# Kernel optimization log

Hardware: AMD Instinct MI355X
Metric: run time of the kernel (lower is better)

Reference implementation:

```python
import jax, jax.numpy as jnp
import numpy as np

N_QUBITS = 12
N_LAYERS = 5
DIM = 1 << N_QUBITS            # 4096
N3 = 3 * N_QUBITS              # 36 params per rotation layer
N_PARAM = N3 * (N_LAYERS + 1)  # 216
BATCH = 1024
# he_std * lrmul with gain=sqrt(2), use_wscale=True, lrmul=1 -> w_mul = sqrt(2/5), init_std = 1
W_SCALE = (2.0 ** 0.5) * (5.0 ** -0.5)
TWO_PI = 2.0 * np.pi

CNOT = jnp.array([[1, 0, 0, 0],
                  [0, 1, 0, 0],
                  [0, 0, 0, 1],
                  [0, 0, 1, 0]], dtype=jnp.complex64)


def setup_inputs() -> dict:
    key = jax.random.key(0)
    k1, k2 = jax.random.split(key)
    x = jax.random.normal(k1, (BATCH, DIM), dtype=jnp.float32)
    weight = (jax.random.uniform(k2, (N_PARAM,), dtype=jnp.float32,
                                 minval=0.0, maxval=TWO_PI) * W_SCALE)
    return {"x": x, "weight": weight}


def _rx(t):
    c = jnp.cos(0.5 * t).astype(jnp.complex64)
    s = jnp.sin(0.5 * t).astype(jnp.complex64)
    return jnp.stack([jnp.stack([c, -1j * s]), jnp.stack([-1j * s, c])])


def _ry(t):
    c = jnp.cos(0.5 * t).astype(jnp.complex64)
    s = jnp.sin(0.5 * t).astype(jnp.complex64)
    return jnp.stack([jnp.stack([c, -s]), jnp.stack([s, c])])


def _rz(t):
    e = jnp.exp(-0.5j * t.astype(jnp.complex64))
    z = jnp.zeros((), dtype=jnp.complex64)
    return jnp.stack([jnp.stack([e, z]), jnp.stack([z, jnp.conj(e)])])


def _apply1(state, U, q):
    # state: [B, 2, ..., 2]; apply 2x2 gate U on qubit axis q
    state = jnp.moveaxis(state, 1 + q, -1)
    state = jnp.einsum('ab,...b->...a', U, state)
    return jnp.moveaxis(state, -1, 1 + q)


def _apply2(state, U, q0, q1):
    # apply 4x4 gate U on (control q0, target q1)
    state = jnp.moveaxis(state, (1 + q0, 1 + q1), (-2, -1))
    shp = state.shape
    state = state.reshape(shp[:-2] + (4,))
    state = jnp.einsum('ab,...b->...a', U, state)
    state = state.reshape(shp)
    return jnp.moveaxis(state, (-2, -1), (1 + q0, 1 + q1))


def reference(x, weight):
    # amplitude_encoding (faithful to source: divides by sqrt(norm), norm = ||x||)
    norm = jnp.sqrt(jnp.sum(x * x, axis=-1, keepdims=True))
    psi = (x / jnp.sqrt(norm + 1e-12)).astype(jnp.complex64)
    state = psi.reshape((x.shape[0],) + (2,) * N_QUBITS)

    for l in range(N_LAYERS):
        p = weight[l * N3:(l + 1) * N3].reshape(N_QUBITS, 3)
        # XYZLayer: rx, ry, rz per qubit (fused into one 2x2 per qubit)
        for q in range(N_QUBITS):
            U = _rz(p[q, 2]) @ _ry(p[q, 1]) @ _rx(p[q, 0])
            state = _apply1(state, U, q)
        # ring_of_cnot
        for q in range(N_QUBITS):
            state = _apply2(state, CNOT, q, (q + 1) % N_QUBITS)

    # final YZYLayer: ry, rz, ry per qubit
    p = weight[N_LAYERS * N3:].reshape(N_QUBITS, 3)
    for q in range(N_QUBITS):
        U = _ry(p[q, 2]) @ _rz(p[q, 1]) @ _ry(p[q, 0])
        state = _apply1(state, U, q)

    res = state.reshape(x.shape[0], DIM)
    return jnp.real(res)
```

## Files before the change

### kernel.cpp

```cpp
#include <hip/hip_runtime.h>
#include <math.h>

#define NQ 12
#define NLAYERS 5
#define TPB 256

typedef float v4f __attribute__((ext_vector_type(4)));
typedef short v8s __attribute__((ext_vector_type(8)));

#define MFMA(A, B, C) __builtin_amdgcn_mfma_f32_16x16x32_bf16((A), (B), (C), 0, 0, 0)

__device__ __forceinline__ float2 cmulf(float2 a, float2 b) {
    return make_float2(a.x * b.x - a.y * b.y, a.x * b.y + a.y * b.x);
}
__device__ __forceinline__ float2 caddf(float2 a, float2 b) {
    return make_float2(a.x + b.x, a.y + b.y);
}
__device__ __forceinline__ void mat2mul(const float2 A[4], const float2 B[4], float2 C[4]) {
    C[0] = caddf(cmulf(A[0], B[0]), cmulf(A[1], B[2]));
    C[1] = caddf(cmulf(A[0], B[1]), cmulf(A[1], B[3]));
    C[2] = caddf(cmulf(A[2], B[0]), cmulf(A[3], B[2]));
    C[3] = caddf(cmulf(A[2], B[1]), cmulf(A[3], B[3]));
}

__device__ __forceinline__ v8s pk4(unsigned a, unsigned b, unsigned c, unsigned d) {
    union { unsigned u[4]; v8s s; } x;
    x.u[0] = a; x.u[1] = b; x.u[2] = c; x.u[3] = d;
    return x.s;
}
__device__ __forceinline__ unsigned cvt2(float a, float b) {
    unsigned d;
    asm("v_cvt_pk_bf16_f32 %0, %1, %2" : "=v"(d) : "v"(a), "v"(b));
    return d;
}
__device__ __forceinline__ unsigned packhl_rne(float f) {
    unsigned h = cvt2(f, 0.0f);
    float lo = f - __uint_as_float(h << 16);
    unsigned l = cvt2(lo, 0.0f);
    return h | (l << 16);
}

__device__ __forceinline__ int sx4(int x) { x ^= x >> 1; x ^= x >> 2; return x & 15; }
__device__ __forceinline__ int permR(int row) {
    int s = sx4(row), par = s & 1;
    return ((s ^ (par << 3)) << 8) | (par ? 0xFF : 0);
}
__device__ __forceinline__ int permT(int t) {
    int s = sx4(t), par = s & 1;
    return (par << 11) | (s << 4) | (par ? 0xF : 0);
}
__device__ __forceinline__ int permL(int lo) {
    int s = sx4(lo), par = s & 1;
    return s | (par << 11);
}

__device__ __forceinline__ int slotOf(int k) {
    int v = k >> 4, m = k & 15;
    int vk = v ^ (((v >> 3) ^ (v >> 7)) & 1);
    return (vk << 4) | ((((m >> 2) ^ v) & 3) << 2) | (m & 3);
}

__device__ __forceinline__ void buildW(const float2* gm, int layer, int beta, int tid,
                                       unsigned& wrd, unsigned& wid) {
    const int r = tid >> 4, c = tid & 15;
    float2 u = make_float2(1.f, 0.f);
    #pragma unroll
    for (int bb = 0; bb < 4; ++bb) {
        const float2 e = gm[(layer * 12 + 11 - beta - bb) * 4 + ((r >> bb) & 1) * 2 + ((c >> bb) & 1)];
        u = cmulf(u, e);
    }
    wrd = packhl_rne(u.x);
    wid = packhl_rne(u.y);
}

__device__ __forceinline__ void makeAfrags(const unsigned* wrR, const unsigned* wiR, int af,
                                           v8s& a_crh, v8s& a_crl, v8s& a_cih, v8s& a_cil) {
    const uint4 wr4 = *reinterpret_cast<const uint4*>(wrR + af);
    const uint4 wi4 = *reinterpret_cast<const uint4*>(wiR + af);
    const unsigned NX = 0x80008000u;
    const unsigned SLO = 0x05040100u, SHI = 0x07060302u;
    unsigned n0 = wi4.x ^ NX, n1 = wi4.y ^ NX, n2 = wi4.z ^ NX, n3 = wi4.w ^ NX;
    a_crh = pk4(__builtin_amdgcn_perm(n0, wr4.x, SLO), __builtin_amdgcn_perm(n1, wr4.y, SLO),
                __builtin_amdgcn_perm(n2, wr4.z, SLO), __builtin_amdgcn_perm(n3, wr4.w, SLO));
    a_crl = pk4(__builtin_amdgcn_perm(n0, wr4.x, SHI), __builtin_amdgcn_perm(n1, wr4.y, SHI),
                __builtin_amdgcn_perm(n2, wr4.z, SHI), __builtin_amdgcn_perm(n3, wr4.w, SHI));
    a_cih = pk4(__builtin_amdgcn_perm(wr4.x, wi4.x, SLO), __builtin_amdgcn_perm(wr4.y, wi4.y, SLO),
                __builtin_amdgcn_perm(wr4.z, wi4.z, SLO), __builtin_amdgcn_perm(wr4.w, wi4.w, SLO));
    a_cil = pk4(__builtin_amdgcn_perm(wr4.x, wi4.x, SHI), __builtin_amdgcn_perm(wr4.y, wi4.y, SHI),
                __builtin_amdgcn_perm(wr4.z, wi4.z, SHI), __builtin_amdgcn_perm(wr4.w, wi4.w, SHI));
}

__global__ __launch_bounds__(TPB) void qsim_kernel(const float* __restrict__ x,
                                                   const float* __restrict__ wgt,
                                                   float* __restrict__ out) {
    __shared__ __align__(16) unsigned st[2][4096];
    __shared__ __align__(16) unsigned wrp[2][256];
    __shared__ __align__(16) unsigned wip[2][256];
    __shared__ __align__(16) float2 gmat[288];
    __shared__ float red[4];

    const int tid = threadIdx.x;
    const int lane = tid & 63;
    const int w = tid >> 6;
    const int hl = lane >> 4;
    const int l15 = lane & 15;
    const int b = blockIdx.x;

    if (tid < 72) {
        const int l = tid / NQ;
        const int q = tid % NQ;
        const float* pp = wgt + (l < NLAYERS ? l * (3 * NQ) : NLAYERS * (3 * NQ)) + q * 3;
        float s0, c0, s1, c1, s2, c2;
        sincosf(0.5f * pp[0], &s0, &c0);
        sincosf(0.5f * pp[1], &s1, &c1);
        sincosf(0.5f * pp[2], &s2, &c2);
        float2 U[4], M[4];
        if (l < NLAYERS) {
            float2 RX[4] = { {c0, 0.f}, {0.f, -s0}, {0.f, -s0}, {c0, 0.f} };
            float2 RY[4] = { {c1, 0.f}, {-s1, 0.f}, {s1, 0.f}, {c1, 0.f} };
            float2 RZ[4] = { {c2, -s2}, {0.f, 0.f}, {0.f, 0.f}, {c2, s2} };
            mat2mul(RY, RX, M);
            mat2mul(RZ, M, U);
        } else {
            float2 RY0[4] = { {c0, 0.f}, {-s0, 0.f}, {s0, 0.f}, {c0, 0.f} };
            float2 RZ1[4] = { {c1, -s1}, {0.f, 0.f}, {0.f, 0.f}, {c1, s1} };
            float2 RY2[4] = { {c2, 0.f}, {-s2, 0.f}, {s2, 0.f}, {c2, 0.f} };
            mat2mul(RZ1, RY0, M);
            mat2mul(RY2, M, U);
        }
        gmat[tid * 4 + 0] = U[0];
        gmat[tid * 4 + 1] = U[1];
        gmat[tid * 4 + 2] = U[2];
        gmat[tid * 4 + 3] = U[3];
    }

    const float* xb = x + (size_t)b * 4096;
    float vals[16];
    float ss = 0.f;
    {
        const float4* xv = reinterpret_cast<const float4*>(xb + 16 * tid);
        #pragma unroll
        for (int k = 0; k < 4; ++k) {
            float4 v = xv[k];
            vals[k * 4 + 0] = v.x; vals[k * 4 + 1] = v.y;
            vals[k * 4 + 2] = v.z; vals[k * 4 + 3] = v.w;
            ss += v.x * v.x + v.y * v.y + v.z * v.z + v.w * v.w;
        }
    }
    #pragma unroll
    for (int off = 32; off > 0; off >>= 1) ss += __shfl_down(ss, off, 64);
    if (lane == 0) red[w] = ss;
    __syncthreads();

    const float total = red[0] + red[1] + red[2] + red[3];
    const float inv = 1.0f / sqrtf(sqrtf(total) + 1e-12f);

    const int vkT = tid ^ (((tid >> 3) ^ (tid >> 7)) & 1);
    #pragma unroll
    for (int jq = 0; jq < 4; ++jq) {
        const int base = (vkT << 4) | (((jq ^ tid) & 3) << 2);
        uint4 eq;
        eq.x = cvt2(vals[jq * 4 + 0] * inv, 0.f);
        eq.y = cvt2(vals[jq * 4 + 1] * inv, 0.f);
        eq.z = cvt2(vals[jq * 4 + 2] * inv, 0.f);
        eq.w = cvt2(vals[jq * 4 + 3] * inv, 0.f);
        *reinterpret_cast<uint4*>(&st[0][base]) = eq;
    }

    {
        unsigned wrd, wid;
        buildW(gmat, 0, 0, tid, wrd, wid);
        wrp[0][tid] = wrd; wip[0][tid] = wid;
    }

    const int v0 = (w << 6) | l15;
    const int vk0 = v0 ^ ((((v0 >> 3) ^ (v0 >> 7)) & 1));
    const int rbase = (vk0 << 4) | ((hl ^ (l15 & 3)) << 2);
    const int af = l15 * 16 + 4 * hl;
    int bw[4], pg[4], pt[4];
    const int sgb = slotOf((4 * hl) << 8);
    const int plc = slotOf(permL(l15));
    #pragma unroll
    for (int ti = 0; ti < 4; ++ti) {
        bw[ti] = sgb ^ slotOf((((4 * w + ti) << 4) | l15));
        pt[ti] = plc ^ slotOf(permT(4 * w + ti));
    }
    #pragma unroll
    for (int g = 0; g < 4; ++g) pg[g] = slotOf(permR(4 * hl + g));
    const int obase = ((4 * hl) << 8) | ((4 * w) << 4) | l15;
    float* outp = out + (size_t)b * 4096;

    __syncthreads();

    const v4f z = {0.f, 0.f, 0.f, 0.f};

    #pragma unroll 1
    for (int p = 0; p < 17; ++p) {
        const unsigned* __restrict__ stR = &st[p & 1][0];
        unsigned* __restrict__ stW = &st[(p + 1) & 1][0];

        v8s a_crh, a_crl, a_cih, a_cil;
        makeAfrags(&wrp[p & 1][0], &wip[p & 1][0], af, a_crh, a_crl, a_cih, a_cil);

        const uint4 s0 = *reinterpret_cast<const uint4*>(stR + rbase);
        const uint4 s1 = *reinterpret_cast<const uint4*>(stR + rbase + 256);
        const uint4 s2 = *reinterpret_cast<const uint4*>(stR + rbase + 512);
        const uint4 s3 = *reinterpret_cast<const uint4*>(stR + rbase + 768);

        unsigned ent[4][4];
        #pragma unroll
        for (int ti = 0; ti < 4; ++ti) {
            const uint4 sv = (ti == 0) ? s0 : (ti == 1) ? s1 : (ti == 2) ? s2 : s3;
            const v8s bsv = pk4(sv.x, sv.y, sv.z, sv.w);
            v4f cr = MFMA(a_crl, bsv, z);
            cr = MFMA(a_crh, bsv, cr);
            v4f ci = MFMA(a_cil, bsv, z);
            ci = MFMA(a_cih, bsv, ci);
            #pragma unroll
            for (int g = 0; g < 4; ++g)
                ent[ti][g] = cvt2(cr[g], ci[g]);
        }

        {
            const int pn = p + 1;
            unsigned wrd, wid;
            buildW(gmat, pn / 3, 4 * (pn % 3), tid, wrd, wid);
            wrp[pn & 1][tid] = wrd;
            wip[pn & 1][tid] = wid;
        }

        if (p % 3 == 2) {
            #pragma unroll
            for (int ti = 0; ti < 4; ++ti) {
                #pragma unroll
                for (int g = 0; g < 4; ++g)
                    stW[pg[g] ^ pt[ti]] = ent[ti][g];
            }
        } else {
            #pragma unroll
            for (int ti = 0; ti < 4; ++ti) {
                #pragma unroll
                for (int g = 0; g < 4; ++g)
                    stW[bw[ti] + (g << 8)] = ent[ti][g];
            }
        }
        __syncthreads();
    }

    {
        const unsigned* __restrict__ stR = &st[1][0];
        v8s a_crh, a_crl, a_cih, a_cil;
        makeAfrags(&wrp[1][0], &wip[1][0], af, a_crh, a_crl, a_cih, a_cil);
        #pragma unroll
        for (int ti = 0; ti < 4; ++ti) {
            const uint4 sv = *reinterpret_cast<const uint4*>(stR + rbase + ti * 256);
            const v8s bsv = pk4(sv.x, sv.y, sv.z, sv.w);
            v4f cr = MFMA(a_crl, bsv, z);
            cr = MFMA(a_crh, bsv, cr);
            #pragma unroll
            for (int g = 0; g < 4; ++g)
                outp[obase + (g << 8) + (ti << 4)] = cr[g];
        }
    }
}

extern "C" void kernel_launch(void* const* d_in, const int* in_sizes, int n_in,
                              void* d_out, int out_size, void* d_ws, size_t ws_size,
                              hipStream_t stream) {
    const float* x = (const float*)d_in[0];
    const float* wgt = (const float*)d_in[1];
    float* out = (float*)d_out;
    qsim_kernel<<<dim3(1024), dim3(TPB), 0, stream>>>(x, wgt, out);
}
```

Measured before the change: 35.80 us.

## Precompute packed gate matrices in a prep kernel and prefetch from global

Moves the per-block trig and 16x16 gate-matrix construction into a single-block prep kernel that writes all 18 packed bf16 matrices to workspace. The main kernel then loads each matrix fragment straight from global (L2-resident) memory, prefetching the next stage's fragment during the current stage. This removes the redundant per-block sincos and buildW work and the LDS traffic for the weight matrices. In exchange it adds a second kernel launch with a serial dependency, plus global-load latency inside the stage loop.

```diff
diff --git a/kernel.cpp b/kernel.cpp
--- a/kernel.cpp
+++ b/kernel.cpp
@@ -73,10 +73,8 @@
     wid = packhl_rne(u.y);
 }
 
-__device__ __forceinline__ void makeAfrags(const unsigned* wrR, const unsigned* wiR, int af,
+__device__ __forceinline__ void makeAfrags(uint4 wr4, uint4 wi4,
                                            v8s& a_crh, v8s& a_crl, v8s& a_cih, v8s& a_cil) {
-    const uint4 wr4 = *reinterpret_cast<const uint4*>(wrR + af);
-    const uint4 wi4 = *reinterpret_cast<const uint4*>(wiR + af);
     const unsigned NX = 0x80008000u;
     const unsigned SLO = 0x05040100u, SHI = 0x07060302u;
     unsigned n0 = wi4.x ^ NX, n1 = wi4.y ^ NX, n2 = wi4.z ^ NX, n3 = wi4.w ^ NX;
@@ -90,22 +88,10 @@
                 __builtin_amdgcn_perm(wr4.z, wi4.z, SHI), __builtin_amdgcn_perm(wr4.w, wi4.w, SHI));
 }
 
-__global__ __launch_bounds__(TPB) void qsim_kernel(const float* __restrict__ x,
-                                                   const float* __restrict__ wgt,
-                                                   float* __restrict__ out) {
-    __shared__ __align__(16) unsigned st[2][4096];
-    __shared__ __align__(16) unsigned wrp[2][256];
-    __shared__ __align__(16) unsigned wip[2][256];
-    __shared__ __align__(16) float2 gmat[288];
-    __shared__ float red[4];
-
+__global__ __launch_bounds__(TPB) void wprep_kernel(const float* __restrict__ wgt,
+                                                    unsigned* __restrict__ ws) {
+    __shared__ float2 gmat[288];
     const int tid = threadIdx.x;
-    const int lane = tid & 63;
-    const int w = tid >> 6;
-    const int hl = lane >> 4;
-    const int l15 = lane & 15;
-    const int b = blockIdx.x;
-
     if (tid < 72) {
         const int l = tid / NQ;
         const int q = tid % NQ;
@@ -133,6 +119,28 @@
         gmat[tid * 4 + 2] = U[2];
         gmat[tid * 4 + 3] = U[3];
     }
+    __syncthreads();
+    #pragma unroll 1
+    for (int p = 0; p < 18; ++p) {
+        unsigned wrd, wid;
+        buildW(gmat, p / 3, 4 * (p % 3), tid, wrd, wid);
+        ws[p * 256 + tid] = wrd;
+        ws[18 * 256 + p * 256 + tid] = wid;
+    }
+}
+
+__global__ __launch_bounds__(TPB) void qsim_kernel(const float* __restrict__ x,
+                                                   const unsigned* __restrict__ ws,
+                                                   float* __restrict__ out) {
+    __shared__ __align__(16) unsigned st[2][4096];
+    __shared__ float red[4];
+
+    const int tid = threadIdx.x;
+    const int lane = tid & 63;
+    const int w = tid >> 6;
+    const int hl = lane >> 4;
+    const int l15 = lane & 15;
+    const int b = blockIdx.x;
 
     const float* xb = x + (size_t)b * 4096;
     float vals[16];
@@ -167,12 +175,6 @@
         *reinterpret_cast<uint4*>(&st[0][base]) = eq;
     }
 
-    {
-        unsigned wrd, wid;
-        buildW(gmat, 0, 0, tid, wrd, wid);
-        wrp[0][tid] = wrd; wip[0][tid] = wid;
-    }
-
     const int v0 = (w << 6) | l15;
     const int vk0 = v0 ^ ((((v0 >> 3) ^ (v0 >> 7)) & 1));
     const int rbase = (vk0 << 4) | ((hl ^ (l15 & 3)) << 2);
@@ -190,6 +192,12 @@
     const int obase = ((4 * hl) << 8) | ((4 * w) << 4) | l15;
     float* outp = out + (size_t)b * 4096;
 
+    const unsigned* gWr = ws;
+    const unsigned* gWi = ws + 18 * 256;
+
+    uint4 wrC = *reinterpret_cast<const uint4*>(gWr + af);
+    uint4 wiC = *reinterpret_cast<const uint4*>(gWi + af);
+
     __syncthreads();
 
     const v4f z = {0.f, 0.f, 0.f, 0.f};
@@ -199,13 +207,16 @@
         const unsigned* __restrict__ stR = &st[p & 1][0];
         unsigned* __restrict__ stW = &st[(p + 1) & 1][0];
 
-        v8s a_crh, a_crl, a_cih, a_cil;
-        makeAfrags(&wrp[p & 1][0], &wip[p & 1][0], af, a_crh, a_crl, a_cih, a_cil);
-
         const uint4 s0 = *reinterpret_cast<const uint4*>(stR + rbase);
         const uint4 s1 = *reinterpret_cast<const uint4*>(stR + rbase + 256);
         const uint4 s2 = *reinterpret_cast<const uint4*>(stR + rbase + 512);
         const uint4 s3 = *reinterpret_cast<const uint4*>(stR + rbase + 768);
+
+        const uint4 wrN = *reinterpret_cast<const uint4*>(gWr + (p + 1) * 256 + af);
+        const uint4 wiN = *reinterpret_cast<const uint4*>(gWi + (p + 1) * 256 + af);
+
+        v8s a_crh, a_crl, a_cih, a_cil;
+        makeAfrags(wrC, wiC, a_crh, a_crl, a_cih, a_cil);
 
         unsigned ent[4][4];
         #pragma unroll
@@ -221,14 +232,6 @@
                 ent[ti][g] = cvt2(cr[g], ci[g]);
         }
 
-        {
-            const int pn = p + 1;
-            unsigned wrd, wid;
-            buildW(gmat, pn / 3, 4 * (pn % 3), tid, wrd, wid);
-            wrp[pn & 1][tid] = wrd;
-            wip[pn & 1][tid] = wid;
-        }
-
         if (p % 3 == 2) {
             #pragma unroll
             for (int ti = 0; ti < 4; ++ti) {
@@ -245,12 +248,14 @@
             }
         }
         __syncthreads();
+
+        wrC = wrN; wiC = wiN;
     }
 
     {
         const unsigned* __restrict__ stR = &st[1][0];
         v8s a_crh, a_crl, a_cih, a_cil;
-        makeAfrags(&wrp[1][0], &wip[1][0], af, a_crh, a_crl, a_cih, a_cil);
+        makeAfrags(wrC, wiC, a_crh, a_crl, a_cih, a_cil);
         #pragma unroll
         for (int ti = 0; ti < 4; ++ti) {
             const uint4 sv = *reinterpret_cast<const uint4*>(stR + rbase + ti * 256);
@@ -270,5 +275,7 @@
     const float* x = (const float*)d_in[0];
     const float* wgt = (const float*)d_in[1];
     float* out = (float*)d_out;
-    qsim_kernel<<<dim3(1024), dim3(TPB), 0, stream>>>(x, wgt, out);
-}
+    unsigned* ws = (unsigned*)d_ws;
+    wprep_kernel<<<dim3(1), dim3(TPB), 0, stream>>>(wgt, ws);
+    qsim_kernel<<<dim3(1024), dim3(TPB), 0, stream>>>(x, ws, out);
+}
```

Result: no change. 35.16 us (-1.8%).
